# Optimization experiments

Measured on AMD Instinct MI355X. Metric: run time of the kernel, lower is better.

The kernel has to match this reference:

```python
import jax, jax.numpy as jnp
import numpy as np
import math

B, L, E, H = 4, 2048, 1024, 16
HD = E // H
SIGMA = 10.0
ATTN_BIAS = 0.1  # source bug: dropout_p=0.1 is passed as attn_mask and added to scores


def setup_inputs() -> dict:
    key = jax.random.key(0)
    ks = jax.random.split(key, 6)
    return {
        "query": jax.random.normal(ks[0], (B, L, E), jnp.float32),
        "key": jax.random.normal(ks[1], (B, L, E), jnp.float32),
        "value": jax.random.normal(ks[2], (B, L, E), jnp.float32),
        "gauss": jax.random.uniform(ks[3], (B * H // 2, L), jnp.float32),
        "in_proj_weight": jax.random.normal(ks[4], (3 * E, E), jnp.float32) * (1.0 / math.sqrt(E)),
        "in_proj_bias": jnp.zeros((3 * E,), jnp.float32),
        "out_proj_weight": jax.random.normal(ks[5], (E, E), jnp.float32) * (1.0 / math.sqrt(E)),
        "out_proj_bias": jnp.zeros((E,), jnp.float32),
    }


def reference(query, key, value, gauss, in_proj_weight, in_proj_bias,
              out_proj_weight, out_proj_bias):
    # packed in-projection (q,k,v distinct tensors -> chunk weights in 3)
    wq, wk, wv = jnp.split(in_proj_weight, 3, axis=0)   # each [E, E]
    bq, bk, bv = jnp.split(in_proj_bias, 3, axis=0)
    q = query @ wq.T + bq          # [B, L, E]
    k = key @ wk.T + bk
    v = value @ wv.T + bv

    def split_heads(x):            # [B, L, E] -> [B*H, L, HD], index = b*H + h
        return x.reshape(B, L, H, HD).transpose(0, 2, 1, 3).reshape(B * H, L, HD)

    q, k, v = split_heads(q), split_heads(k), split_heads(v)
    q = q * (1.0 / math.sqrt(HD))

    attn = jnp.einsum("bnd,bmd->bnm", q, k) + ATTN_BIAS   # [B*H, L, L]
    gw = jnp.exp(-gauss * SIGMA)                          # [B*H//2, L]
    # even/odd batch rows share the same gaussian row -> pairwise broadcast
    attn = (attn.reshape(B * H // 2, 2, L, L) * gw[:, None, None, :]).reshape(B * H, L, L)
    attn = jax.nn.softmax(attn, axis=-1)

    out = jnp.einsum("bnm,bmd->bnd", attn, v)             # [B*H, L, HD]
    out = out.reshape(B, H, L, HD).transpose(0, 2, 1, 3).reshape(B, L, E)
    return out @ out_proj_weight.T + out_proj_bias        # [B, L, E]
```

## Files before the change

### kernel.cpp

```cpp
#include <hip/hip_runtime.h>
#include <stdint.h>
#include <stddef.h>


typedef __attribute__((ext_vector_type(8))) short bf16x8;
typedef __attribute__((ext_vector_type(4))) float f32x4;

__device__ __forceinline__ unsigned short f2b(float f) {
  unsigned int u = __builtin_bit_cast(unsigned int, f);
  u += 0x7FFFu + ((u >> 16) & 1u);
  return (unsigned short)(u >> 16);
}
__device__ __forceinline__ bf16x8 cvt8(f32x4 a, f32x4 b) {
  bf16x8 r;
#pragma unroll
  for (int i = 0; i < 4; ++i) { r[i] = (short)f2b(a[i]); r[4 + i] = (short)f2b(b[i]); }
  return r;
}
__device__ __forceinline__ bf16x8 pk8(f32x4 a, f32x4 b) {
  union { bf16x8 v; unsigned int w[4]; } u;
  asm("v_cvt_pk_bf16_f32 %0, %1, %2" : "=v"(u.w[0]) : "v"(a[0]), "v"(a[1]));
  asm("v_cvt_pk_bf16_f32 %0, %1, %2" : "=v"(u.w[1]) : "v"(a[2]), "v"(a[3]));
  asm("v_cvt_pk_bf16_f32 %0, %1, %2" : "=v"(u.w[2]) : "v"(b[0]), "v"(b[1]));
  asm("v_cvt_pk_bf16_f32 %0, %1, %2" : "=v"(u.w[3]) : "v"(b[2]), "v"(b[3]));
  return u.v;
}
__device__ __forceinline__ float fexp2(float x) { return __builtin_amdgcn_exp2f(x); }

#define GLD16(gp, lp) __builtin_amdgcn_global_load_lds( \
  (const __attribute__((address_space(1))) void*)(gp), \
  (__attribute__((address_space(3))) void*)(lp), 16, 0, 0)

#define FBAR() do { \
  asm volatile("" ::: "memory"); \
  __builtin_amdgcn_sched_barrier(0); \
  __builtin_amdgcn_s_barrier(); \
  __builtin_amdgcn_sched_barrier(0); \
  asm volatile("" ::: "memory"); \
} while (0)

__global__ void __launch_bounds__(256) gw_exp_kernel(const float* __restrict__ g,
                                                     float* __restrict__ gtab,
                                                     float* __restrict__ btab, int n) {
  int i = blockIdx.x * 256 + threadIdx.x;
  if (i < n) {
    const float e = __expf(g[i] * -10.0f) * 1.44269504f;
    gtab[i] = e;
    btab[i] = 0.1f * e;
  }
}

__global__ void __launch_bounds__(256) conv_bf16_kernel(
    const float* __restrict__ q, const float* __restrict__ k, const float* __restrict__ v,
    const float* __restrict__ w1, const float* __restrict__ w2,
    unsigned short* __restrict__ dst)
{
  const size_t i = ((size_t)blockIdx.x * 256 + threadIdx.x) * 8;
  const int seg = (int)(i >> 20);
  const float* s; size_t off;
  if (seg < 8)       { s = q;  off = i; }
  else if (seg < 16) { s = k;  off = i - ((size_t)8 << 20); }
  else if (seg < 24) { s = v;  off = i - ((size_t)16 << 20); }
  else if (seg < 27) { s = w1; off = i - ((size_t)24 << 20); }
  else               { s = w2; off = i - ((size_t)27 << 20); }
  const f32x4 a = *(const f32x4*)(s + off);
  const f32x4 b = *(const f32x4*)(s + off + 4);
  *(bf16x8*)(dst + i) = cvt8(a, b);
}

template<int EPI>
__global__ void __launch_bounds__(512, 2) gemm8p(
    const unsigned short* __restrict__ A0, const unsigned short* __restrict__ Bw,
    const float* __restrict__ bias, const float* __restrict__ gtab,
    unsigned short* __restrict__ Qo, unsigned short* __restrict__ Ko,
    unsigned short* __restrict__ Vto, float* __restrict__ Co,
    int N, int K, int nTN)
{
  const int nwg = gridDim.x;
  const int cpx = nwg >> 3;
  const int bid2 = (blockIdx.x & 7) * cpx + (blockIdx.x >> 3);
  const int tm = bid2 / nTN, tn = bid2 % nTN;

  const unsigned short* A = A0;
  if (EPI == 0) A = A0 + (size_t)(tn >> 2) * 8388608;

  __shared__ __align__(16) char lds[2][49152];

  const int tid = threadIdx.x;
  const int w = tid >> 6, l = tid & 63;
  const int lr = l & 15, lg = l >> 4;
  const int wm = w >> 2, wn = w & 3;
  const size_t Kz = (size_t)K;

  const int r0 = tid >> 3;
  const int sch = (((tid & 7) ^ ((tid >> 3) & 7)) << 3);
  const size_t arow0 = (size_t)(tm * 128 + r0);
  const size_t brow0 = (size_t)(tn * 256 + r0);

  auto stA = [&](int s, int k0) {
    GLD16(A + arow0 * Kz + k0 + sch,        &lds[s][tid * 16]);
    GLD16(A + (arow0 + 64) * Kz + k0 + sch, &lds[s][8192 + tid * 16]);
  };
  auto stB = [&](int s, int h, int k0) {
    const size_t rb = brow0 + h * 128;
    GLD16(Bw + rb * Kz + k0 + sch,        &lds[s][16384 + h * 16384 + tid * 16]);
    GLD16(Bw + (rb + 64) * Kz + k0 + sch, &lds[s][16384 + h * 16384 + 8192 + tid * 16]);
  };

  int offA[4][2], offB[4][2];
#pragma unroll
  for (int m = 0; m < 4; ++m) {
    const int ra = wm * 64 + m * 16 + lr;
#pragma unroll
    for (int kk = 0; kk < 2; ++kk)
      offA[m][kk] = ra * 128 + ((((kk << 2) | lg) ^ (ra & 7)) << 4);
  }
#pragma unroll
  for (int n = 0; n < 4; ++n) {
    const int br = wn * 64 + n * 16 + lr;
    const int lrow = br & 127;
#pragma unroll
    for (int kk = 0; kk < 2; ++kk)
      offB[n][kk] = 16384 + (br >> 7) * 16384 + lrow * 128 +
                    ((((kk << 2) | lg) ^ (lrow & 7)) << 4);
  }

  f32x4 acc[4][4];
  const f32x4 zero = {0.f, 0.f, 0.f, 0.f};
#pragma unroll
  for (int i = 0; i < 4; ++i)
#pragma unroll
    for (int j = 0; j < 4; ++j) acc[i][j] = zero;

  bf16x8 af[2][2], bf[4][2];

  auto loadA = [&](const char* Ls, int mh) {
#pragma unroll
    for (int mm = 0; mm < 2; ++mm)
#pragma unroll
      for (int kk = 0; kk < 2; ++kk)
        af[mm][kk] = *(const bf16x8*)(Ls + offA[mh * 2 + mm][kk]);
  };
  auto loadB = [&](const char* Ls) {
#pragma unroll
    for (int n = 0; n < 4; ++n)
#pragma unroll
      for (int kk = 0; kk < 2; ++kk)
        bf[n][kk] = *(const bf16x8*)(Ls + offB[n][kk]);
  };
  auto mfmaq = [&](int mh) {
    asm volatile("s_waitcnt lgkmcnt(0)" ::: "memory");
    __builtin_amdgcn_sched_barrier(0);
    __builtin_amdgcn_s_setprio(1);
#pragma unroll
    for (int mm = 0; mm < 2; ++mm)
#pragma unroll
      for (int n = 0; n < 4; ++n) {
        f32x4 a = acc[mh * 2 + mm][n];
        a = __builtin_amdgcn_mfma_f32_16x16x32_bf16(af[mm][0], bf[n][0], a, 0, 0, 0);
        a = __builtin_amdgcn_mfma_f32_16x16x32_bf16(af[mm][1], bf[n][1], a, 0, 0, 0);
        acc[mh * 2 + mm][n] = a;
      }
    __builtin_amdgcn_s_setprio(0);
  };

  const char* L0 = (const char*)lds[0];
  const char* L1 = (const char*)lds[1];

  stA(0, 0); stB(0, 0, 0); stB(0, 1, 0);

  const int NI = K / 128;
  for (int i = 0; i < NI; ++i) {
    const int k1 = i * 128 + 64;
    const int k2 = i * 128 + 128;
    stA(1, k1); stB(1, 0, k1);
    asm volatile("s_waitcnt vmcnt(4)" ::: "memory");
    FBAR();
    loadA(L0, 0); loadB(L0);
    mfmaq(0);
    FBAR();
    stB(1, 1, k1);
    loadA(L0, 1);
    mfmaq(1);
    FBAR();
    if (i + 1 < NI) {
      stA(0, k2); stB(0, 0, k2);
      asm volatile("s_waitcnt vmcnt(4)" ::: "memory");
    } else {
      asm volatile("s_waitcnt vmcnt(0)" ::: "memory");
    }
    FBAR();
    loadA(L1, 0); loadB(L1);
    mfmaq(0);
    FBAR();
    if (i + 1 < NI) stB(0, 1, k2);
    loadA(L1, 1);
    mfmaq(1);
    FBAR();
  }

  if (EPI == 0 && (tn >> 2) == 2) {
    __syncthreads();
    char* T = &lds[0][0];
#pragma unroll
    for (int n = 0; n < 4; ++n) {
      const int cnl = wn * 64 + n * 16 + lr;
      const float bv = bias[tn * 256 + cnl];
      const int sw = (cnl & 7) << 4;
#pragma unroll
      for (int m = 0; m < 4; ++m)
#pragma unroll
        for (int r = 0; r < 4; ++r) {
          const int rml = wm * 64 + m * 16 + lg * 4 + r;
          *(unsigned short*)(T + cnl * 256 + ((rml * 2) ^ sw)) = f2b(acc[m][n][r] + bv);
        }
    }
    __syncthreads();
    const int bbase = (tm >> 4) * 16 + (tn - 8) * 4;
    const size_t ncol = (size_t)(tm & 15) * 128;
#pragma unroll
    for (int rep = 0; rep < 8; ++rep) {
      const int U = rep * 512 + tid;
      const int row = U >> 4;
      const int un = U & 15;
      const bf16x8 vv = *(const bf16x8*)(T + row * 256 + ((un * 16) ^ ((row & 7) << 4)));
      const int bh = bbase + (row >> 6);
      const int d = row & 63;
      *(bf16x8*)(Vto + ((size_t)bh * 64 + d) * 2048 + ncol + un * 8) = vv;
    }
  } else {
#pragma unroll
    for (int n = 0; n < 4; ++n) {
      const int cn = tn * 256 + wn * 64 + n * 16 + lr;
      const float bv = bias[cn];
      const int j = cn & 1023;
      const float* gK = nullptr;
      if constexpr (EPI == 0) {
        if ((tn >> 2) == 1) {
          const int bh_ = (tm >> 4) * 16 + (j >> 6);
          gK = gtab + (size_t)(bh_ >> 1) * 2048;
        }
      }
#pragma unroll
      for (int m = 0; m < 4; ++m) {
        const int rm0 = tm * 128 + wm * 64 + m * 16 + lg * 4;
        f32x4 g4;
        if constexpr (EPI == 0) {
          if (gK) g4 = *(const f32x4*)&gK[rm0 & 2047];
        }
#pragma unroll
        for (int r = 0; r < 4; ++r) {
          const int rm = rm0 + r;
          const float val = acc[m][n][r] + bv;
          if constexpr (EPI == 0) {
            const int bh = (rm >> 11) * 16 + (j >> 6);
            const int d = j & 63;
            const int nr = rm & 2047;
            if ((tn >> 2) == 0) Qo[((size_t)bh * 2048 + nr) * 64 + d] = f2b(val * 0.125f);
            else                Ko[((size_t)bh * 2048 + nr) * 64 + d] = f2b(val * g4[r]);
          } else {
            Co[(size_t)rm * N + cn] = val;
          }
        }
      }
    }
  }
}

__global__ void __launch_bounds__(256, 2) attn_kernel(
    const unsigned short* __restrict__ Q, const unsigned short* __restrict__ Kf,
    const unsigned short* __restrict__ Vt, const float* __restrict__ btab,
    unsigned short* __restrict__ O)
{
  const int bid2 = (blockIdx.x & 7) * 64 + (blockIdx.x >> 3);
  const int bh = bid2 >> 3;
  const int qb = bid2 & 7;
  const int tid = threadIdx.x;
  const int w = tid >> 6, l = tid & 63;
  const int lr = l & 15, lg = l >> 4;

  __shared__ __align__(16) unsigned short Kl[2][64 * 64];
  __shared__ __align__(16) unsigned short Vl[2][64 * 64];

  const int qrow = qb * 256 + w * 64 + lr;
  const unsigned short* qp = &Q[((size_t)bh * 2048 + qrow) * 64];
  bf16x8 aq[4][2];
#pragma unroll
  for (int st = 0; st < 4; ++st) {
    aq[st][0] = *(const bf16x8*)&qp[st * 16 * 64 + lg * 8];
    aq[st][1] = *(const bf16x8*)&qp[st * 16 * 64 + 32 + lg * 8];
  }

  const f32x4 zero = {0.f, 0.f, 0.f, 0.f};
  f32x4 accO[4][4];
  f32x4 lsum[4];
#pragma unroll
  for (int st = 0; st < 4; ++st) {
    lsum[st] = zero;
#pragma unroll
    for (int dt = 0; dt < 4; ++dt) accO[st][dt] = zero;
  }

  const short oneb = (short)0x3F80;
  const bf16x8 vones = {oneb, oneb, oneb, oneb, oneb, oneb, oneb, oneb};

  int off[4][2];
#pragma unroll
  for (int mt = 0; mt < 4; ++mt)
#pragma unroll
    for (int c = 0; c < 2; ++c) {
      const int rr = mt * 16 + lr;
      off[mt][c] = rr * 128 + ((((c << 2) + lg) ^ (rr & 7)) << 4);
    }

  const int rr0 = w * 8 + (l >> 3);
  const int cc = ((l & 7) ^ (rr0 & 7)) * 8;
  const int kk0 = (rr0 & 35) | ((rr0 & 12) << 1) | ((rr0 & 16) >> 2);
  const unsigned short* kSrc = &Kf[((size_t)bh * 2048 + kk0) * 64 + cc];
  const unsigned short* vSrc = &Vt[((size_t)bh * 64 + rr0) * 2048 + cc];

  auto stageKV = [&](int buf) {
    GLD16(kSrc,             &Kl[buf][w * 512]);
    GLD16(kSrc + 32 * 64,   &Kl[buf][(w + 4) * 512]);
    GLD16(vSrc,             &Vl[buf][w * 512]);
    GLD16(vSrc + 32 * 2048, &Vl[buf][(w + 4) * 512]);
    kSrc += 64 * 64;
    vSrc += 64;
  };

  const float* brow = &btab[(size_t)(bh >> 1) * 2048];

  stageKV(0);
  for (int t = 0; t < 32; ++t) {
    __syncthreads();
    if (t + 1 < 32) stageKV((t + 1) & 1);
    const char* kl = (const char*)Kl[t & 1];
    const char* vl = (const char*)Vl[t & 1];

    bf16x8 ap[4][2];
#pragma unroll
    for (int half = 0; half < 2; ++half) {
      f32x4 s[4][2];
      __builtin_amdgcn_s_setprio(1);
#pragma unroll
      for (int mh = 0; mh < 2; ++mh) {
        const int mt = half * 2 + mh;
        const bf16x8 bk0 = *(const bf16x8*)(kl + off[mt][0]);
        const bf16x8 bk1 = *(const bf16x8*)(kl + off[mt][1]);
        const f32x4 b4 = *(const f32x4*)&brow[t * 64 + (half << 5) + (lg << 3) + (mh << 2)];
#pragma unroll
        for (int st = 0; st < 4; ++st) {
          f32x4 a = __builtin_amdgcn_mfma_f32_16x16x32_bf16(bk0, aq[st][0], b4, 0, 0, 0);
          a = __builtin_amdgcn_mfma_f32_16x16x32_bf16(bk1, aq[st][1], a, 0, 0, 0);
          s[st][mh] = a;
        }
      }
      __builtin_amdgcn_s_setprio(0);
#pragma unroll
      for (int st = 0; st < 4; ++st) {
#pragma unroll
        for (int mh = 0; mh < 2; ++mh)
#pragma unroll
          for (int r = 0; r < 4; ++r) s[st][mh][r] = fexp2(s[st][mh][r]);
        ap[st][half] = pk8(s[st][0], s[st][1]);
      }
    }

    __builtin_amdgcn_s_setprio(1);
#pragma unroll
    for (int st = 0; st < 4; ++st) {
      lsum[st] = __builtin_amdgcn_mfma_f32_16x16x32_bf16(ap[st][0], vones, lsum[st], 0, 0, 0);
      lsum[st] = __builtin_amdgcn_mfma_f32_16x16x32_bf16(ap[st][1], vones, lsum[st], 0, 0, 0);
    }
#pragma unroll
    for (int dt = 0; dt < 4; ++dt) {
      const bf16x8 bv0 = *(const bf16x8*)(vl + off[dt][0]);
      const bf16x8 bv1 = *(const bf16x8*)(vl + off[dt][1]);
#pragma unroll
      for (int st = 0; st < 4; ++st) {
        f32x4 a = accO[st][dt];
        a = __builtin_amdgcn_mfma_f32_16x16x32_bf16(ap[st][0], bv0, a, 0, 0, 0);
        a = __builtin_amdgcn_mfma_f32_16x16x32_bf16(ap[st][1], bv1, a, 0, 0, 0);
        accO[st][dt] = a;
      }
    }
    __builtin_amdgcn_s_setprio(0);
  }

  const int oc0 = (bh & 15) * 64;
#pragma unroll
  for (int st = 0; st < 4; ++st) {
    const int orow0 = (bh >> 4) * 2048 + qb * 256 + w * 64 + st * 16 + lg * 4;
    f32x4 rc;
#pragma unroll
    for (int r = 0; r < 4; ++r) rc[r] = 1.0f / lsum[st][r];
#pragma unroll
    for (int dt = 0; dt < 4; ++dt)
#pragma unroll
      for (int r = 0; r < 4; ++r)
        O[(size_t)(orow0 + r) * 1024 + oc0 + dt * 16 + lr] = f2b(accO[st][dt][r] * rc[r]);
  }
}

extern "C" void kernel_launch(void* const* d_in, const int* in_sizes, int n_in,
                              void* d_out, int out_size, void* d_ws, size_t ws_size,
                              hipStream_t stream) {
  (void)in_sizes; (void)n_in; (void)out_size; (void)ws_size;
  const float* query = (const float*)d_in[0];
  const float* key_  = (const float*)d_in[1];
  const float* value = (const float*)d_in[2];
  const float* gauss = (const float*)d_in[3];
  const float* ipw   = (const float*)d_in[4];
  const float* ipb   = (const float*)d_in[5];
  const float* opw   = (const float*)d_in[6];
  const float* opb   = (const float*)d_in[7];

  char* ws = (char*)d_ws;
  unsigned short* Xbf = (unsigned short*)ws;
  unsigned short* W1  = Xbf + ((size_t)24 << 20);
  unsigned short* W2  = Xbf + ((size_t)27 << 20);
  unsigned short* AO  = Xbf;
  unsigned short* Qf  = Xbf + ((size_t)28 << 20);
  unsigned short* Kf  = Qf + (size_t)64 * 2048 * 64;
  unsigned short* Vt  = Kf + (size_t)64 * 2048 * 64;
  float*          gtab = (float*)(Vt + (size_t)64 * 2048 * 64);
  float*          btab = gtab + 32 * 2048;

  gw_exp_kernel<<<256, 256, 0, stream>>>(gauss, gtab, btab, 32 * 2048);

  conv_bf16_kernel<<<14336, 256, 0, stream>>>(query, key_, value, ipw, opw, Xbf);

  gemm8p<0><<<64 * 12, 512, 0, stream>>>(
      Xbf, W1, ipb, gtab, Qf, Kf, Vt, nullptr, 3072, 1024, 12);

  attn_kernel<<<512, 256, 0, stream>>>(Qf, Kf, Vt, btab, AO);

  gemm8p<1><<<64 * 4, 512, 0, stream>>>(
      AO, W2, opb, nullptr, nullptr, nullptr, nullptr, (float*)d_out, 1024, 1024, 4);
}
```

Baseline: 197.3 us.

## Fuse fp32-to-bf16 activation conversion into the QKV projection GEMM A-loads

The QKV GEMM now reads fp32 query/key/value straight from global memory into registers, packs them to bf16 and writes them into LDS itself. The standalone conversion kernel only converts the weights. This removes a full fp32 read plus bf16 write and re-read of the 24M activation elements, and shrinks the workspace. In exchange the A-operand loads can no longer use direct global-to-LDS copies and must pass through registers with extra waitcnt stalls. Each GEMM block also reads twice the bytes for A, since fp32 is wider than bf16.

```diff
diff --git a/kernel.cpp b/kernel.cpp
--- a/kernel.cpp
+++ b/kernel.cpp
@@ -51,18 +51,13 @@
 }
 
 __global__ void __launch_bounds__(256) conv_bf16_kernel(
-    const float* __restrict__ q, const float* __restrict__ k, const float* __restrict__ v,
     const float* __restrict__ w1, const float* __restrict__ w2,
     unsigned short* __restrict__ dst)
 {
   const size_t i = ((size_t)blockIdx.x * 256 + threadIdx.x) * 8;
-  const int seg = (int)(i >> 20);
   const float* s; size_t off;
-  if (seg < 8)       { s = q;  off = i; }
-  else if (seg < 16) { s = k;  off = i - ((size_t)8 << 20); }
-  else if (seg < 24) { s = v;  off = i - ((size_t)16 << 20); }
-  else if (seg < 27) { s = w1; off = i - ((size_t)24 << 20); }
-  else               { s = w2; off = i - ((size_t)27 << 20); }
+  if (i < ((size_t)3 << 20)) { s = w1; off = i; }
+  else                       { s = w2; off = i - ((size_t)3 << 20); }
   const f32x4 a = *(const f32x4*)(s + off);
   const f32x4 b = *(const f32x4*)(s + off + 4);
   *(bf16x8*)(dst + i) = cvt8(a, b);
@@ -70,7 +65,9 @@
 
 template<int EPI>
 __global__ void __launch_bounds__(512, 2) gemm8p(
-    const unsigned short* __restrict__ A0, const unsigned short* __restrict__ Bw,
+    const float* __restrict__ Aq, const float* __restrict__ Ak,
+    const float* __restrict__ Av, const unsigned short* __restrict__ Abf,
+    const unsigned short* __restrict__ Bw,
     const float* __restrict__ bias, const float* __restrict__ gtab,
     unsigned short* __restrict__ Qo, unsigned short* __restrict__ Ko,
     unsigned short* __restrict__ Vto, float* __restrict__ Co,
@@ -81,9 +78,6 @@
   const int bid2 = (blockIdx.x & 7) * cpx + (blockIdx.x >> 3);
   const int tm = bid2 / nTN, tn = bid2 % nTN;
 
-  const unsigned short* A = A0;
-  if (EPI == 0) A = A0 + (size_t)(tn >> 2) * 8388608;
-
   __shared__ __align__(16) char lds[2][49152];
 
   const int tid = threadIdx.x;
@@ -93,18 +87,33 @@
   const size_t Kz = (size_t)K;
 
   const int r0 = tid >> 3;
-  const int sch = (((tid & 7) ^ ((tid >> 3) & 7)) << 3);
+  const int e0 = (((tid & 7) ^ ((tid >> 3) & 7)) << 3);
   const size_t arow0 = (size_t)(tm * 128 + r0);
   const size_t brow0 = (size_t)(tn * 256 + r0);
 
-  auto stA = [&](int s, int k0) {
-    GLD16(A + arow0 * Kz + k0 + sch,        &lds[s][tid * 16]);
-    GLD16(A + (arow0 + 64) * Kz + k0 + sch, &lds[s][8192 + tid * 16]);
+  const float* Af = (tn >> 2) == 0 ? Aq : ((tn >> 2) == 1 ? Ak : Av);
+
+  f32x4 ar0[4], ar1[4];
+  auto ldA = [&](f32x4* ar, int k0) {
+    const float* pa = Af + arow0 * Kz + k0 + e0;
+    const float* pb = Af + (arow0 + 64) * Kz + k0 + e0;
+    ar[0] = *(const __attribute__((address_space(1))) f32x4*)pa;
+    ar[1] = *(const __attribute__((address_space(1))) f32x4*)(pa + 4);
+    ar[2] = *(const __attribute__((address_space(1))) f32x4*)pb;
+    ar[3] = *(const __attribute__((address_space(1))) f32x4*)(pb + 4);
+  };
+  auto wrA = [&](f32x4* ar, int s) {
+    *(bf16x8*)&lds[s][tid * 16]        = pk8(ar[0], ar[1]);
+    *(bf16x8*)&lds[s][8192 + tid * 16] = pk8(ar[2], ar[3]);
+  };
+  auto stAbf = [&](int s, int k0) {
+    GLD16(Abf + arow0 * Kz + k0 + e0,        &lds[s][tid * 16]);
+    GLD16(Abf + (arow0 + 64) * Kz + k0 + e0, &lds[s][8192 + tid * 16]);
   };
   auto stB = [&](int s, int h, int k0) {
     const size_t rb = brow0 + h * 128;
-    GLD16(Bw + rb * Kz + k0 + sch,        &lds[s][16384 + h * 16384 + tid * 16]);
-    GLD16(Bw + (rb + 64) * Kz + k0 + sch, &lds[s][16384 + h * 16384 + 8192 + tid * 16]);
+    GLD16(Bw + rb * Kz + k0 + e0,        &lds[s][16384 + h * 16384 + tid * 16]);
+    GLD16(Bw + (rb + 64) * Kz + k0 + e0, &lds[s][16384 + h * 16384 + 8192 + tid * 16]);
   };
 
   int offA[4][2], offB[4][2];
@@ -167,14 +176,22 @@
   const char* L0 = (const char*)lds[0];
   const char* L1 = (const char*)lds[1];
 
-  stA(0, 0); stB(0, 0, 0); stB(0, 1, 0);
+  if constexpr (EPI == 0) { ldA(ar0, 0); } else { stAbf(0, 0); }
+  stB(0, 0, 0); stB(0, 1, 0);
 
   const int NI = K / 128;
   for (int i = 0; i < NI; ++i) {
     const int k1 = i * 128 + 64;
     const int k2 = i * 128 + 128;
-    stA(1, k1); stB(1, 0, k1);
-    asm volatile("s_waitcnt vmcnt(4)" ::: "memory");
+    if constexpr (EPI == 0) {
+      ldA(ar1, k1); stB(1, 0, k1);
+      asm volatile("s_waitcnt vmcnt(6)" ::: "memory");
+      wrA(ar0, 0);
+      asm volatile("s_waitcnt lgkmcnt(0)" ::: "memory");
+    } else {
+      stAbf(1, k1); stB(1, 0, k1);
+      asm volatile("s_waitcnt vmcnt(4)" ::: "memory");
+    }
     FBAR();
     loadA(L0, 0); loadB(L0);
     mfmaq(0);
@@ -183,11 +200,22 @@
     loadA(L0, 1);
     mfmaq(1);
     FBAR();
-    if (i + 1 < NI) {
-      stA(0, k2); stB(0, 0, k2);
-      asm volatile("s_waitcnt vmcnt(4)" ::: "memory");
+    if constexpr (EPI == 0) {
+      if (i + 1 < NI) {
+        ldA(ar0, k2); stB(0, 0, k2);
+        asm volatile("s_waitcnt vmcnt(6)" ::: "memory");
+      } else {
+        asm volatile("s_waitcnt vmcnt(0)" ::: "memory");
+      }
+      wrA(ar1, 1);
+      asm volatile("s_waitcnt lgkmcnt(0)" ::: "memory");
     } else {
-      asm volatile("s_waitcnt vmcnt(0)" ::: "memory");
+      if (i + 1 < NI) {
+        stAbf(0, k2); stB(0, 0, k2);
+        asm volatile("s_waitcnt vmcnt(4)" ::: "memory");
+      } else {
+        asm volatile("s_waitcnt vmcnt(0)" ::: "memory");
+      }
     }
     FBAR();
     loadA(L1, 0); loadB(L1);
@@ -416,25 +444,26 @@
   const float* opb   = (const float*)d_in[7];
 
   char* ws = (char*)d_ws;
-  unsigned short* Xbf = (unsigned short*)ws;
-  unsigned short* W1  = Xbf + ((size_t)24 << 20);
-  unsigned short* W2  = Xbf + ((size_t)27 << 20);
-  unsigned short* AO  = Xbf;
-  unsigned short* Qf  = Xbf + ((size_t)28 << 20);
-  unsigned short* Kf  = Qf + (size_t)64 * 2048 * 64;
-  unsigned short* Vt  = Kf + (size_t)64 * 2048 * 64;
-  float*          gtab = (float*)(Vt + (size_t)64 * 2048 * 64);
+  unsigned short* W1  = (unsigned short*)ws;
+  unsigned short* W2  = W1 + ((size_t)3 << 20);
+  unsigned short* AO  = W1 + ((size_t)4 << 20);
+  unsigned short* Qf  = W1 + ((size_t)12 << 20);
+  unsigned short* Kf  = Qf + ((size_t)8 << 20);
+  unsigned short* Vt  = Kf + ((size_t)8 << 20);
+  float*          gtab = (float*)(Vt + ((size_t)8 << 20));
   float*          btab = gtab + 32 * 2048;
 
   gw_exp_kernel<<<256, 256, 0, stream>>>(gauss, gtab, btab, 32 * 2048);
 
-  conv_bf16_kernel<<<14336, 256, 0, stream>>>(query, key_, value, ipw, opw, Xbf);
+  conv_bf16_kernel<<<2048, 256, 0, stream>>>(ipw, opw, W1);
 
   gemm8p<0><<<64 * 12, 512, 0, stream>>>(
-      Xbf, W1, ipb, gtab, Qf, Kf, Vt, nullptr, 3072, 1024, 12);
+      query, key_, value, nullptr, W1, ipb, gtab,
+      Qf, Kf, Vt, nullptr, 3072, 1024, 12);
 
   attn_kernel<<<512, 256, 0, stream>>>(Qf, Kf, Vt, btab, AO);
 
   gemm8p<1><<<64 * 4, 512, 0, stream>>>(
-      AO, W2, opb, nullptr, nullptr, nullptr, nullptr, (float*)d_out, 1024, 1024, 4);
-}
+      nullptr, nullptr, nullptr, AO, W2, opb, nullptr,
+      nullptr, nullptr, nullptr, (float*)d_out, 1024, 1024, 4);
+}
```

Result: faster. 189.3 us, median of 2 (-4.1%).
